# Kernel optimization log

Measured on AMD Instinct MI355X. Metric: run time of the kernel, lower is better.

Reference implementation:

```python
import jax, jax.numpy as jnp
import numpy as np


def _coord1d(n):
    # make_coord: grid-center coordinates in (-1, 1)
    return -1.0 + 1.0 / n + (2.0 / n) * jnp.arange(n, dtype=jnp.float32)


def _conv1x1(x, w, b):
    # 1x1 conv == channel matmul. x: [B,C,H,W], w: [O,C], b: [O]
    return jnp.einsum('bchw,oc->bohw', x, w) + b[None, :, None, None]


def setup_inputs() -> dict:
    key = jax.random.key(0)
    ks = jax.random.split(key, 8)
    B, C, h, w = 2, 64, 96, 96
    d = 256
    Cin = (C + 2) * 4 + 2  # 266
    s = lambda k, shp, fan: (jax.random.normal(k, shp, jnp.float32) / np.sqrt(fan)).astype(jnp.float32)
    return {
        'feat': jax.random.normal(ks[0], (B, C, h, w), jnp.float32),
        'w00': s(ks[1], (d, Cin), Cin), 'b00': jnp.zeros((d,), jnp.float32),
        'w1': s(ks[2], (d, d), d), 'b1': jnp.zeros((d,), jnp.float32),
        'w2': s(ks[3], (3, d), d), 'b2': jnp.zeros((3,), jnp.float32),
        'ws1': s(ks[4], (C, C), C), 'bs1': jnp.zeros((C,), jnp.float32),
        'ws2': s(ks[5], (3, C), C), 'bs2': jnp.zeros((3,), jnp.float32),
        'target_h': 384, 'target_w': 384,
    }


def reference(feat, w00, b00, w1, b1, w2, b2, ws1, bs1, ws2, bs2, target_h, target_w):
    B, C, h, w = feat.shape
    H, W = int(target_h), int(target_w)
    # HR query coordinates, shared across batch. cy along height (dim0), cx along width (dim1)
    cy = jnp.broadcast_to(_coord1d(H)[:, None], (H, W))
    cx = jnp.broadcast_to(_coord1d(W)[None, :], (H, W))
    rx = 1.0 / h  # = 2/h/2, half-pixel radius along height
    ry = 1.0 / w
    eps_shift = 1e-6

    def nearest(c, n):
        # grid_sample nearest, align_corners=False: unnormalize then round (half-to-even, as nearbyint)
        u = ((c + 1.0) * n - 1.0) / 2.0
        return jnp.clip(jnp.round(u).astype(jnp.int32), 0, n - 1)

    rel_coords, feat_s, areas = [], [], []
    for vx in (-1.0, 1.0):
        for vy in (-1.0, 1.0):
            sy = jnp.clip(cy + vx * rx + eps_shift, -1.0 + 1e-6, 1.0 - 1e-6)
            sx = jnp.clip(cx + vy * ry + eps_shift, -1.0 + 1e-6, 1.0 - 1e-6)
            iy = nearest(sy, h)  # [H,W]
            ix = nearest(sx, w)
            feat_s.append(feat[:, :, iy, ix])  # [B,C,H,W] gather
            # nearest-sampled LR pixel-center coords (what grid_sample(pos_lr,...) returns)
            old_y = -1.0 + 1.0 / h + (2.0 / h) * iy.astype(jnp.float32)
            old_x = -1.0 + 1.0 / w + (2.0 / w) * ix.astype(jnp.float32)
            rel_y = (cy - old_y) * h
            rel_x = (cx - old_x) * w
            rel_coords.append(jnp.stack([rel_y, rel_x], 0))  # [2,H,W]
            areas.append(jnp.abs(rel_y * rel_x) + 1e-9)

    tot = areas[0] + areas[1] + areas[2] + areas[3]
    # LIIF area swap: 0<->3, 1<->2
    areas = [areas[3], areas[2], areas[1], areas[0]]
    feat_s = [f * (a / tot)[None, None] for f, a in zip(feat_s, areas)]

    scale_h, scale_w = H / h, W / w
    cell_h = (2.0 / H) * max(scale_h / 4.0, 1.0) * h
    cell_w = (2.0 / W) * max(scale_w / 4.0, 1.0) * w
    rel_cell = jnp.broadcast_to(
        jnp.array([cell_h, cell_w], jnp.float32)[None, :, None, None], (B, 2, H, W))
    rels = jnp.broadcast_to(jnp.concatenate(rel_coords, 0)[None], (B, 8, H, W))
    grid = jnp.concatenate([rels, *feat_s, rel_cell], axis=1)  # [B,266,H,W]

    x = _conv1x1(grid, w00, b00)
    ret = _conv1x1(jax.nn.gelu(_conv1x1(x, w1, b1), approximate=False), w2, b2)

    # shortcut branch: 1x1 MLP on LR feat, then bilinear border sample at coord
    sc = _conv1x1(jax.nn.relu(_conv1x1(feat, ws1, bs1)), ws2, bs2)  # [B,3,h,w]
    uy = ((cy + 1.0) * h - 1.0) / 2.0
    ux = ((cx + 1.0) * w - 1.0) / 2.0
    y0 = jnp.floor(uy)
    x0 = jnp.floor(ux)
    wy = uy - y0
    wx = ux - x0
    y0i = jnp.clip(y0.astype(jnp.int32), 0, h - 1)
    y1i = jnp.clip(y0.astype(jnp.int32) + 1, 0, h - 1)
    x0i = jnp.clip(x0.astype(jnp.int32), 0, w - 1)
    x1i = jnp.clip(x0.astype(jnp.int32) + 1, 0, w - 1)
    samp = (sc[:, :, y0i, x0i] * ((1 - wy) * (1 - wx))[None, None]
            + sc[:, :, y0i, x1i] * ((1 - wy) * wx)[None, None]
            + sc[:, :, y1i, x0i] * (wy * (1 - wx))[None, None]
            + sc[:, :, y1i, x1i] * (wy * wx)[None, None])
    return ret + samp
```

## Files before the change

kernel.cpp:

```cpp
#include <hip/hip_runtime.h>

typedef __bf16 bf16x8 __attribute__((ext_vector_type(8)));
typedef __bf16 bf16x4 __attribute__((ext_vector_type(4)));
typedef float f32x4 __attribute__((ext_vector_type(4)));

namespace {
constexpr int Bn = 2, Cn = 64, hn = 96, wn = 96, Hn = 384, Wn = 384;
constexpr int CIN = 266;
constexpr int TM = 64;
constexpr int SP = 296;
constexpr int L1_FRAGS = 9 * 16 * 64;
constexpr int L2_FRAGS = 8 * 16 * 64;
constexpr int L3_FRAGS = 8 * 64;
constexpr int N_FRAGS = L1_FRAGS + L2_FRAGS + L3_FRAGS;
constexpr int SC_OFF_BYTES = N_FRAGS * 16;
constexpr int B1EFF_OFF_BYTES = SC_OFF_BYTES + Bn * 3 * hn * wn * 4;
constexpr int FEATT_OFF_BYTES = B1EFF_OFF_BYTES + 1024;
constexpr int FRAG_BLOCKS = N_FRAGS / 256;
constexpr int SC_BLOCKS = (Bn * hn * wn) / 256;
}

__global__ void prep_all(const float* __restrict__ w00, const float* __restrict__ w1,
                         const float* __restrict__ w2, const float* __restrict__ b00,
                         const float* __restrict__ b1,
                         const float* __restrict__ feat, const float* __restrict__ ws1,
                         const float* __restrict__ bs1, const float* __restrict__ ws2,
                         const float* __restrict__ bs2,
                         __bf16* __restrict__ wb, float* __restrict__ b1eff,
                         float* __restrict__ sc, float* __restrict__ featT)
{
    const int bid = blockIdx.x;
    if (bid < FRAG_BLOCKS) {
        const int f = bid * 256 + threadIdx.x;
        bf16x8 v;
        if (f < L1_FRAGS) {
            const int k0 = f >> 10;
            const int mb = (f >> 6) & 15;
            const int l  = f & 63;
            const int m  = mb * 16 + (l & 15);
            const int kb = k0 * 32 + (l >> 4) * 8;
#pragma unroll
            for (int j = 0; j < 8; j++)
                v[j] = (kb + j < CIN) ? (__bf16)w00[m * CIN + kb + j] : (__bf16)0.f;
        } else if (f < L1_FRAGS + L2_FRAGS) {
            const int g = f - L1_FRAGS;
            const int k0 = g >> 10;
            const int mb = (g >> 6) & 15;
            const int l  = g & 63;
            const int m  = mb * 16 + (l & 15);
            const int kb = k0 * 32 + (l >> 4) * 8;
#pragma unroll
            for (int j = 0; j < 8; j++) v[j] = (__bf16)w1[m * 256 + kb + j];
        } else {
            const int g = f - (L1_FRAGS + L2_FRAGS);
            const int k0 = g >> 6;
            const int l  = g & 63;
            const int m  = l & 15;
            const int kb = k0 * 32 + (l >> 4) * 8;
#pragma unroll
            for (int j = 0; j < 8; j++)
                v[j] = (m < 3) ? (__bf16)w2[m * 256 + kb + j] : (__bf16)0.f;
        }
        *(bf16x8*)(wb + f * 8) = v;
        return;
    }
    if (bid == FRAG_BLOCKS) {
        __shared__ float cb[256];
        const int o = threadIdx.x;
        cb[o] = b00[o] + 0.5f * (w00[o * CIN + 264] + w00[o * CIN + 265]);
        __syncthreads();
        float v = b1[o];
#pragma unroll 4
        for (int k = 0; k < 256; k++) v = fmaf(w1[o * 256 + k], cb[k], v);
        b1eff[o] = v;
        return;
    }
    const int t = (bid - FRAG_BLOCKS - 1) * 256 + threadIdx.x;
    if (t >= Bn * hn * wn) return;
    const int b = t / (hn * wn);
    const int yx = t % (hn * wn);
    const float* fp = feat + b * Cn * hn * wn + yx;
    float f[Cn];
#pragma unroll
    for (int c = 0; c < Cn; c++) f[c] = fp[c * hn * wn];
    {
        float* ft = featT + t * Cn;
#pragma unroll
        for (int c4 = 0; c4 < Cn / 4; c4++)
            *(f32x4*)&ft[c4 * 4] =
                (f32x4){f[4 * c4], f[4 * c4 + 1], f[4 * c4 + 2], f[4 * c4 + 3]};
    }
    float o0 = bs2[0], o1 = bs2[1], o2 = bs2[2];
#pragma unroll 1
    for (int co = 0; co < Cn; co += 4) {
        float v0 = bs1[co], v1 = bs1[co + 1], v2 = bs1[co + 2], v3 = bs1[co + 3];
        const float* wr = ws1 + co * Cn;
#pragma unroll
        for (int ci = 0; ci < Cn; ci++) {
            const float fv = f[ci];
            v0 = fmaf(wr[ci], fv, v0);
            v1 = fmaf(wr[Cn + ci], fv, v1);
            v2 = fmaf(wr[2 * Cn + ci], fv, v2);
            v3 = fmaf(wr[3 * Cn + ci], fv, v3);
        }
        v0 = fmaxf(v0, 0.f); v1 = fmaxf(v1, 0.f); v2 = fmaxf(v2, 0.f); v3 = fmaxf(v3, 0.f);
#pragma unroll
        for (int u = 0; u < 4; u++) {
            const float vv = (u == 0) ? v0 : (u == 1) ? v1 : (u == 2) ? v2 : v3;
            o0 = fmaf(ws2[co + u], vv, o0);
            o1 = fmaf(ws2[Cn + co + u], vv, o1);
            o2 = fmaf(ws2[2 * Cn + co + u], vv, o2);
        }
    }
    sc[(b * 3 + 0) * hn * wn + yx] = o0;
    sc[(b * 3 + 1) * hn * wn + yx] = o1;
    sc[(b * 3 + 2) * hn * wn + yx] = o2;
}

__device__ __forceinline__ float gelu_fast(float x) {
    const float d0 = -2.302118074f;
    const float d1 = -0.1029453754f;
    float t = x * x;
    float a = x * fmaf(t, d1, d0);
    float e = __builtin_amdgcn_exp2f(a);
    return x * __builtin_amdgcn_rcpf(1.f + e);
}

__device__ __forceinline__ bf16x4 pack4(f32x4 x) {
    bf16x4 v;
    v[0] = (__bf16)x[0]; v[1] = (__bf16)x[1]; v[2] = (__bf16)x[2]; v[3] = (__bf16)x[3];
    return v;
}


#define MF(A, B, C) __builtin_amdgcn_mfma_f32_16x16x32_bf16((A), (B), (C), 0, 0, 0)

#define GSTEP(k0, W0, W1, W2, W3) do {                                          \
    const bf16x8 g0 = *(const bf16x8*)&Abuf[     lane16][(k0) * 32 + quad * 8]; \
    const bf16x8 g1 = *(const bf16x8*)&Abuf[16 + lane16][(k0) * 32 + quad * 8]; \
    const bf16x8 g2 = *(const bf16x8*)&Abuf[32 + lane16][(k0) * 32 + quad * 8]; \
    const bf16x8 g3 = *(const bf16x8*)&Abuf[48 + lane16][(k0) * 32 + quad * 8]; \
    a00 = MF(W0, g0, a00); a01 = MF(W1, g0, a01); a02 = MF(W2, g0, a02); a03 = MF(W3, g0, a03); \
    a10 = MF(W0, g1, a10); a11 = MF(W1, g1, a11); a12 = MF(W2, g1, a12); a13 = MF(W3, g1, a13); \
    a20 = MF(W0, g2, a20); a21 = MF(W1, g2, a21); a22 = MF(W2, g2, a22); a23 = MF(W3, g2, a23); \
    a30 = MF(W0, g3, a30); a31 = MF(W1, g3, a31); a32 = MF(W2, g3, a32); a33 = MF(W3, g3, a33); \
} while (0)

#define LDW(W0, W1, W2, W3, src, kk) do {             \
    W0 = (src)[((kk) * 16 + mb0 + 0) * 64 + lane];    \
    W1 = (src)[((kk) * 16 + mb0 + 1) * 64 + lane];    \
    W2 = (src)[((kk) * 16 + mb0 + 2) * 64 + lane];    \
    W3 = (src)[((kk) * 16 + mb0 + 3) * 64 + lane];    \
} while (0)

#define ZACC4(n) a##n##0 = zf; a##n##1 = zf; a##n##2 = zf; a##n##3 = zf

__global__ __launch_bounds__(256, 3) void liif_main(
    const float* __restrict__ featT, const float* __restrict__ b1eff,
    const float* __restrict__ b2v, const __bf16* __restrict__ wb,
    const float* __restrict__ sc, float* __restrict__ out)
{
    __shared__ __align__(16) __bf16 Abuf[TM][SP];

    const int t = threadIdx.x;
    const int wv = t >> 6;
    const int lane = t & 63;
    const int lane16 = lane & 15;
    const int quad = lane >> 4;
    const int mb0 = wv * 4;

    constexpr int NWG = Bn * Hn * (Wn / TM);
    const int lt = (blockIdx.x & 7) * (NWG / 8) + (blockIdx.x >> 3);
    constexpr int TPR = Wn / TM;
    const int tx = lt % TPR;
    const int Y = (lt / TPR) % Hn;
    const int b = lt / (TPR * Hn);
    const int X0 = tx * TM;

    const float cy = -1.f + 1.f / Hn + (2.f / Hn) * (float)Y;

    const bf16x8* wf1 = (const bf16x8*)wb;
    const bf16x8* wf2 = wf1 + L1_FRAGS;
    const bf16x8* w2f = wf1 + (L1_FRAGS + L2_FRAGS);

    bf16x8 wE0, wE1, wE2, wE3, wO0, wO1, wO2, wO3;
    LDW(wE0, wE1, wE2, wE3, wf1, 0);
    LDW(wO0, wO1, wO2, wO3, wf1, 1);

    {
        const int p = lane;
        const int j = wv;
        const int X = X0 + p;
        const float cx = -1.f + 1.f / Wn + (2.f / Wn) * (float)X;
        float relyv[2], relxv[2];
        int iyy[2], ixx[2];
#pragma unroll
        for (int c2 = 0; c2 < 2; c2++) {
            const float v = c2 ? 1.f : -1.f;
            float sy = fminf(fmaxf(cy + v * (1.f / hn) + 1e-6f, -1.f + 1e-6f), 1.f - 1e-6f);
            float uy = ((sy + 1.f) * hn - 1.f) * 0.5f;
            int iy = min(max((int)rintf(uy), 0), hn - 1);
            float oy = -1.f + 1.f / hn + (2.f / hn) * (float)iy;
            relyv[c2] = (cy - oy) * hn; iyy[c2] = iy;
            float sx = fminf(fmaxf(cx + v * (1.f / wn) + 1e-6f, -1.f + 1e-6f), 1.f - 1e-6f);
            float ux = ((sx + 1.f) * wn - 1.f) * 0.5f;
            int ix = min(max((int)rintf(ux), 0), wn - 1);
            float ox = -1.f + 1.f / wn + (2.f / wn) * (float)ix;
            relxv[c2] = (cx - ox) * wn; ixx[c2] = ix;
        }
        float area[4];
#pragma unroll
        for (int c = 0; c < 4; c++)
            area[c] = fabsf(relyv[(c >> 1) & 1] * relxv[c & 1]) + 1e-9f;
        const float tot = area[0] + area[1] + area[2] + area[3];
        const float wj = area[3 - j] / tot;

        if (j == 0) {
            bf16x8 v;
#pragma unroll
            for (int c = 0; c < 4; c++) {
                v[2 * c] = (__bf16)relyv[(c >> 1) & 1];
                v[2 * c + 1] = (__bf16)relxv[c & 1];
            }
            *(bf16x8*)&Abuf[p][0] = v;
        }
        const float* fb = featT + ((b * hn + iyy[(j >> 1) & 1]) * wn + ixx[j & 1]) * Cn;
#pragma unroll
        for (int c8 = 0; c8 < 8; c8++) {
            const f32x4 u0 = *(const f32x4*)&fb[c8 * 8];
            const f32x4 u1 = *(const f32x4*)&fb[c8 * 8 + 4];
            bf16x8 v;
            v[0] = (__bf16)(u0[0] * wj); v[1] = (__bf16)(u0[1] * wj);
            v[2] = (__bf16)(u0[2] * wj); v[3] = (__bf16)(u0[3] * wj);
            v[4] = (__bf16)(u1[0] * wj); v[5] = (__bf16)(u1[1] * wj);
            v[6] = (__bf16)(u1[2] * wj); v[7] = (__bf16)(u1[3] * wj);
            *(bf16x8*)&Abuf[p][8 + 64 * j + c8 * 8] = v;
        }
        if (j == 3) {
            bf16x8 z;
#pragma unroll
            for (int cc = 0; cc < 8; cc++) z[cc] = (__bf16)0.f;
            *(bf16x8*)&Abuf[p][264] = z;
            *(bf16x8*)&Abuf[p][272] = z;
            *(bf16x8*)&Abuf[p][280] = z;
        }
    }
    __syncthreads();

    const f32x4 zf = (f32x4){0.f, 0.f, 0.f, 0.f};
    f32x4 a00, a01, a02, a03, a10, a11, a12, a13;
    f32x4 a20, a21, a22, a23, a30, a31, a32, a33;
    ZACC4(0); ZACC4(1); ZACC4(2); ZACC4(3);

    GSTEP(0, wE0, wE1, wE2, wE3); LDW(wE0, wE1, wE2, wE3, wf1, 2);
    GSTEP(1, wO0, wO1, wO2, wO3); LDW(wO0, wO1, wO2, wO3, wf1, 3);
    GSTEP(2, wE0, wE1, wE2, wE3); LDW(wE0, wE1, wE2, wE3, wf1, 4);
    GSTEP(3, wO0, wO1, wO2, wO3); LDW(wO0, wO1, wO2, wO3, wf1, 5);
    GSTEP(4, wE0, wE1, wE2, wE3); LDW(wE0, wE1, wE2, wE3, wf1, 6);
    GSTEP(5, wO0, wO1, wO2, wO3); LDW(wO0, wO1, wO2, wO3, wf1, 7);
    GSTEP(6, wE0, wE1, wE2, wE3); LDW(wE0, wE1, wE2, wE3, wf1, 8);
    GSTEP(7, wO0, wO1, wO2, wO3); LDW(wO0, wO1, wO2, wO3, wf2, 0);
    GSTEP(8, wE0, wE1, wE2, wE3); LDW(wE0, wE1, wE2, wE3, wf2, 1);

    __syncthreads();
    {
        const int ch0 = mb0 * 16 + quad * 4;
        *(bf16x4*)&Abuf[     lane16][ch0     ] = pack4(a00);
        *(bf16x4*)&Abuf[16 + lane16][ch0     ] = pack4(a10);
        *(bf16x4*)&Abuf[32 + lane16][ch0     ] = pack4(a20);
        *(bf16x4*)&Abuf[48 + lane16][ch0     ] = pack4(a30);
        *(bf16x4*)&Abuf[     lane16][ch0 + 16] = pack4(a01);
        *(bf16x4*)&Abuf[16 + lane16][ch0 + 16] = pack4(a11);
        *(bf16x4*)&Abuf[32 + lane16][ch0 + 16] = pack4(a21);
        *(bf16x4*)&Abuf[48 + lane16][ch0 + 16] = pack4(a31);
        *(bf16x4*)&Abuf[     lane16][ch0 + 32] = pack4(a02);
        *(bf16x4*)&Abuf[16 + lane16][ch0 + 32] = pack4(a12);
        *(bf16x4*)&Abuf[32 + lane16][ch0 + 32] = pack4(a22);
        *(bf16x4*)&Abuf[48 + lane16][ch0 + 32] = pack4(a32);
        *(bf16x4*)&Abuf[     lane16][ch0 + 48] = pack4(a03);
        *(bf16x4*)&Abuf[16 + lane16][ch0 + 48] = pack4(a13);
        *(bf16x4*)&Abuf[32 + lane16][ch0 + 48] = pack4(a23);
        *(bf16x4*)&Abuf[48 + lane16][ch0 + 48] = pack4(a33);
    }
    __syncthreads();

    ZACC4(0); ZACC4(1); ZACC4(2); ZACC4(3);

    GSTEP(0, wO0, wO1, wO2, wO3); LDW(wO0, wO1, wO2, wO3, wf2, 2);
    GSTEP(1, wE0, wE1, wE2, wE3); LDW(wE0, wE1, wE2, wE3, wf2, 3);
    GSTEP(2, wO0, wO1, wO2, wO3); LDW(wO0, wO1, wO2, wO3, wf2, 4);
    GSTEP(3, wE0, wE1, wE2, wE3); LDW(wE0, wE1, wE2, wE3, wf2, 5);
    GSTEP(4, wO0, wO1, wO2, wO3); LDW(wO0, wO1, wO2, wO3, wf2, 6);
    GSTEP(5, wE0, wE1, wE2, wE3); LDW(wE0, wE1, wE2, wE3, wf2, 7);
    GSTEP(6, wO0, wO1, wO2, wO3); wO0 = w2f[0 * 64 + lane];
    GSTEP(7, wE0, wE1, wE2, wE3); wE0 = w2f[1 * 64 + lane];

    __syncthreads();
    {
        const int ch0 = mb0 * 16 + quad * 4;
        const f32x4 bi0 = *(const f32x4*)&b1eff[ch0];
        const f32x4 bi1 = *(const f32x4*)&b1eff[ch0 + 16];
        const f32x4 bi2 = *(const f32x4*)&b1eff[ch0 + 32];
        const f32x4 bi3 = *(const f32x4*)&b1eff[ch0 + 48];
#define GEL4(x, bi) { bf16x4 v; v[0] = (__bf16)gelu_fast((x)[0] + (bi)[0]); \
        v[1] = (__bf16)gelu_fast((x)[1] + (bi)[1]); \
        v[2] = (__bf16)gelu_fast((x)[2] + (bi)[2]); \
        v[3] = (__bf16)gelu_fast((x)[3] + (bi)[3]); vv = v; }
        bf16x4 vv;
        GEL4(a00, bi0); *(bf16x4*)&Abuf[     lane16][ch0     ] = vv;
        GEL4(a10, bi0); *(bf16x4*)&Abuf[16 + lane16][ch0     ] = vv;
        GEL4(a20, bi0); *(bf16x4*)&Abuf[32 + lane16][ch0     ] = vv;
        GEL4(a30, bi0); *(bf16x4*)&Abuf[48 + lane16][ch0     ] = vv;
        GEL4(a01, bi1); *(bf16x4*)&Abuf[     lane16][ch0 + 16] = vv;
        GEL4(a11, bi1); *(bf16x4*)&Abuf[16 + lane16][ch0 + 16] = vv;
        GEL4(a21, bi1); *(bf16x4*)&Abuf[32 + lane16][ch0 + 16] = vv;
        GEL4(a31, bi1); *(bf16x4*)&Abuf[48 + lane16][ch0 + 16] = vv;
        GEL4(a02, bi2); *(bf16x4*)&Abuf[     lane16][ch0 + 32] = vv;
        GEL4(a12, bi2); *(bf16x4*)&Abuf[16 + lane16][ch0 + 32] = vv;
        GEL4(a22, bi2); *(bf16x4*)&Abuf[32 + lane16][ch0 + 32] = vv;
        GEL4(a32, bi2); *(bf16x4*)&Abuf[48 + lane16][ch0 + 32] = vv;
        GEL4(a03, bi3); *(bf16x4*)&Abuf[     lane16][ch0 + 48] = vv;
        GEL4(a13, bi3); *(bf16x4*)&Abuf[16 + lane16][ch0 + 48] = vv;
        GEL4(a23, bi3); *(bf16x4*)&Abuf[32 + lane16][ch0 + 48] = vv;
        GEL4(a33, bi3); *(bf16x4*)&Abuf[48 + lane16][ch0 + 48] = vv;
#undef GEL4
    }
    __syncthreads();

    f32x4 acc3 = zf;
#define YF(k0) (*(const bf16x8*)&Abuf[wv * 16 + lane16][(k0) * 32 + quad * 8])
    acc3 = MF(wO0, YF(0), acc3); wO0 = w2f[2 * 64 + lane];
    acc3 = MF(wE0, YF(1), acc3); wE0 = w2f[3 * 64 + lane];
    acc3 = MF(wO0, YF(2), acc3); wO0 = w2f[4 * 64 + lane];
    acc3 = MF(wE0, YF(3), acc3); wE0 = w2f[5 * 64 + lane];
    acc3 = MF(wO0, YF(4), acc3); wO0 = w2f[6 * 64 + lane];
    acc3 = MF(wE0, YF(5), acc3); wE0 = w2f[7 * 64 + lane];
    acc3 = MF(wO0, YF(6), acc3);
    acc3 = MF(wE0, YF(7), acc3);
#undef YF

    if (quad == 0) {
        const int pix = wv * 16 + lane16;
        const int X = X0 + pix;
        const float uy = ((cy + 1.f) * hn - 1.f) * 0.5f;
        const float fy = floorf(uy);
        const float wy = uy - fy;
        const int y0i = min(max((int)fy, 0), hn - 1);
        const int y1i = min(max((int)fy + 1, 0), hn - 1);
        const float cx = -1.f + 1.f / Wn + (2.f / Wn) * (float)X;
        const float ux = ((cx + 1.f) * wn - 1.f) * 0.5f;
        const float fx = floorf(ux);
        const float wx = ux - fx;
        const int x0i = min(max((int)fx, 0), wn - 1);
        const int x1i = min(max((int)fx + 1, 0), wn - 1);
        const float w00b = (1.f - wy) * (1.f - wx), w01b = (1.f - wy) * wx;
        const float w10b = wy * (1.f - wx), w11b = wy * wx;
#pragma unroll
        for (int r = 0; r < 3; r++) {
            const float* scb = sc + (b * 3 + r) * (hn * wn);
            const float samp = scb[y0i * wn + x0i] * w00b + scb[y0i * wn + x1i] * w01b
                             + scb[y1i * wn + x0i] * w10b + scb[y1i * wn + x1i] * w11b;
            out[((b * 3 + r) * Hn + Y) * Wn + X] = acc3[r] + b2v[r] + samp;
        }
    }
}

extern "C" void kernel_launch(void* const* d_in, const int* in_sizes, int n_in,
                              void* d_out, int out_size, void* d_ws, size_t ws_size,
                              hipStream_t stream)
{
    const float* feat = (const float*)d_in[0];
    const float* w00  = (const float*)d_in[1];
    const float* b00  = (const float*)d_in[2];
    const float* w1   = (const float*)d_in[3];
    const float* b1   = (const float*)d_in[4];
    const float* w2   = (const float*)d_in[5];
    const float* b2   = (const float*)d_in[6];
    const float* ws1  = (const float*)d_in[7];
    const float* bs1  = (const float*)d_in[8];
    const float* ws2  = (const float*)d_in[9];
    const float* bs2  = (const float*)d_in[10];
    float* out = (float*)d_out;

    __bf16* wb    = (__bf16*)d_ws;
    float* scbuf  = (float*)((char*)d_ws + SC_OFF_BYTES);
    float* b1eff  = (float*)((char*)d_ws + B1EFF_OFF_BYTES);
    float* featT  = (float*)((char*)d_ws + FEATT_OFF_BYTES);

    prep_all<<<FRAG_BLOCKS + 1 + SC_BLOCKS, 256, 0, stream>>>(
        w00, w1, w2, b00, b1, feat, ws1, bs1, ws2, bs2, wb, b1eff, scbuf, featT);
    liif_main<<<Bn * Hn * (Wn / TM), 256, 0, stream>>>(featT, b1eff, b2, wb, scbuf, out);
}
```

Baseline: 207.0 us.

## Process two pixel tiles per workgroup, prefetching second tile's gather during first

```diff
diff --git a/kernel.cpp b/kernel.cpp
--- a/kernel.cpp
+++ b/kernel.cpp
@@ -153,7 +153,120 @@
     W3 = (src)[((kk) * 16 + mb0 + 3) * 64 + lane];    \
 } while (0)
 
-#define ZACC4(n) a##n##0 = zf; a##n##1 = zf; a##n##2 = zf; a##n##3 = zf
+#define ZACCALL do { a00 = zf; a01 = zf; a02 = zf; a03 = zf; \
+    a10 = zf; a11 = zf; a12 = zf; a13 = zf;                   \
+    a20 = zf; a21 = zf; a22 = zf; a23 = zf;                   \
+    a30 = zf; a31 = zf; a32 = zf; a33 = zf; } while (0)
+
+#define L1_SEC do {                                                   \
+    GSTEP(0, wE0, wE1, wE2, wE3); LDW(wE0, wE1, wE2, wE3, wf1, 2);    \
+    GSTEP(1, wO0, wO1, wO2, wO3); LDW(wO0, wO1, wO2, wO3, wf1, 3);    \
+    GSTEP(2, wE0, wE1, wE2, wE3); LDW(wE0, wE1, wE2, wE3, wf1, 4);    \
+    GSTEP(3, wO0, wO1, wO2, wO3); LDW(wO0, wO1, wO2, wO3, wf1, 5);    \
+    GSTEP(4, wE0, wE1, wE2, wE3); LDW(wE0, wE1, wE2, wE3, wf1, 6);    \
+    GSTEP(5, wO0, wO1, wO2, wO3); LDW(wO0, wO1, wO2, wO3, wf1, 7);    \
+    GSTEP(6, wE0, wE1, wE2, wE3); LDW(wE0, wE1, wE2, wE3, wf1, 8);    \
+    GSTEP(7, wO0, wO1, wO2, wO3); LDW(wO0, wO1, wO2, wO3, wf2, 0);    \
+    GSTEP(8, wE0, wE1, wE2, wE3); LDW(wE0, wE1, wE2, wE3, wf2, 1);    \
+} while (0)
+
+#define L2_SEC do {                                                   \
+    GSTEP(0, wO0, wO1, wO2, wO3); LDW(wO0, wO1, wO2, wO3, wf2, 2);    \
+    GSTEP(1, wE0, wE1, wE2, wE3); LDW(wE0, wE1, wE2, wE3, wf2, 3);    \
+    GSTEP(2, wO0, wO1, wO2, wO3); LDW(wO0, wO1, wO2, wO3, wf2, 4);    \
+    GSTEP(3, wE0, wE1, wE2, wE3); LDW(wE0, wE1, wE2, wE3, wf2, 5);    \
+    GSTEP(4, wO0, wO1, wO2, wO3); LDW(wO0, wO1, wO2, wO3, wf2, 6);    \
+    GSTEP(5, wE0, wE1, wE2, wE3); LDW(wE0, wE1, wE2, wE3, wf2, 7);    \
+    GSTEP(6, wO0, wO1, wO2, wO3); wO0 = w2f[0 * 64 + lane];           \
+    GSTEP(7, wE0, wE1, wE2, wE3); wE0 = w2f[1 * 64 + lane];           \
+} while (0)
+
+#define YF(k0) (*(const bf16x8*)&Abuf[wv * 16 + lane16][(k0) * 32 + quad * 8])
+#define L3_SEC do {                                                   \
+    acc3 = zf;                                                        \
+    acc3 = MF(wO0, YF(0), acc3); wO0 = w2f[2 * 64 + lane];            \
+    acc3 = MF(wE0, YF(1), acc3); wE0 = w2f[3 * 64 + lane];            \
+    acc3 = MF(wO0, YF(2), acc3); wO0 = w2f[4 * 64 + lane];            \
+    acc3 = MF(wE0, YF(3), acc3); wE0 = w2f[5 * 64 + lane];            \
+    acc3 = MF(wO0, YF(4), acc3); wO0 = w2f[6 * 64 + lane];            \
+    acc3 = MF(wE0, YF(5), acc3); wE0 = w2f[7 * 64 + lane];            \
+    acc3 = MF(wO0, YF(6), acc3);                                      \
+    acc3 = MF(wE0, YF(7), acc3);                                      \
+} while (0)
+
+#define EP1_STORE do {                                                \
+    const int ch0 = mb0 * 16 + quad * 4;                              \
+    *(bf16x4*)&Abuf[     lane16][ch0     ] = pack4(a00);              \
+    *(bf16x4*)&Abuf[16 + lane16][ch0     ] = pack4(a10);              \
+    *(bf16x4*)&Abuf[32 + lane16][ch0     ] = pack4(a20);              \
+    *(bf16x4*)&Abuf[48 + lane16][ch0     ] = pack4(a30);              \
+    *(bf16x4*)&Abuf[     lane16][ch0 + 16] = pack4(a01);              \
+    *(bf16x4*)&Abuf[16 + lane16][ch0 + 16] = pack4(a11);              \
+    *(bf16x4*)&Abuf[32 + lane16][ch0 + 16] = pack4(a21);              \
+    *(bf16x4*)&Abuf[48 + lane16][ch0 + 16] = pack4(a31);              \
+    *(bf16x4*)&Abuf[     lane16][ch0 + 32] = pack4(a02);              \
+    *(bf16x4*)&Abuf[16 + lane16][ch0 + 32] = pack4(a12);              \
+    *(bf16x4*)&Abuf[32 + lane16][ch0 + 32] = pack4(a22);              \
+    *(bf16x4*)&Abuf[48 + lane16][ch0 + 32] = pack4(a32);              \
+    *(bf16x4*)&Abuf[     lane16][ch0 + 48] = pack4(a03);              \
+    *(bf16x4*)&Abuf[16 + lane16][ch0 + 48] = pack4(a13);              \
+    *(bf16x4*)&Abuf[32 + lane16][ch0 + 48] = pack4(a23);              \
+    *(bf16x4*)&Abuf[48 + lane16][ch0 + 48] = pack4(a33);              \
+} while (0)
+
+#define GEL4(x, bi) { bf16x4 v_; v_[0] = (__bf16)gelu_fast((x)[0] + (bi)[0]); \
+    v_[1] = (__bf16)gelu_fast((x)[1] + (bi)[1]); \
+    v_[2] = (__bf16)gelu_fast((x)[2] + (bi)[2]); \
+    v_[3] = (__bf16)gelu_fast((x)[3] + (bi)[3]); vv = v_; }
+
+#define EP2_STORE do {                                                \
+    const int ch0 = mb0 * 16 + quad * 4;                              \
+    const f32x4 bi0 = *(const f32x4*)&b1eff[ch0];                     \
+    const f32x4 bi1 = *(const f32x4*)&b1eff[ch0 + 16];                \
+    const f32x4 bi2 = *(const f32x4*)&b1eff[ch0 + 32];                \
+    const f32x4 bi3 = *(const f32x4*)&b1eff[ch0 + 48];                \
+    bf16x4 vv;                                                        \
+    GEL4(a00, bi0); *(bf16x4*)&Abuf[     lane16][ch0     ] = vv;      \
+    GEL4(a10, bi0); *(bf16x4*)&Abuf[16 + lane16][ch0     ] = vv;      \
+    GEL4(a20, bi0); *(bf16x4*)&Abuf[32 + lane16][ch0     ] = vv;      \
+    GEL4(a30, bi0); *(bf16x4*)&Abuf[48 + lane16][ch0     ] = vv;      \
+    GEL4(a01, bi1); *(bf16x4*)&Abuf[     lane16][ch0 + 16] = vv;      \
+    GEL4(a11, bi1); *(bf16x4*)&Abuf[16 + lane16][ch0 + 16] = vv;      \
+    GEL4(a21, bi1); *(bf16x4*)&Abuf[32 + lane16][ch0 + 16] = vv;      \
+    GEL4(a31, bi1); *(bf16x4*)&Abuf[48 + lane16][ch0 + 16] = vv;      \
+    GEL4(a02, bi2); *(bf16x4*)&Abuf[     lane16][ch0 + 32] = vv;      \
+    GEL4(a12, bi2); *(bf16x4*)&Abuf[16 + lane16][ch0 + 32] = vv;      \
+    GEL4(a22, bi2); *(bf16x4*)&Abuf[32 + lane16][ch0 + 32] = vv;      \
+    GEL4(a32, bi2); *(bf16x4*)&Abuf[48 + lane16][ch0 + 32] = vv;      \
+    GEL4(a03, bi3); *(bf16x4*)&Abuf[     lane16][ch0 + 48] = vv;      \
+    GEL4(a13, bi3); *(bf16x4*)&Abuf[16 + lane16][ch0 + 48] = vv;      \
+    GEL4(a23, bi3); *(bf16x4*)&Abuf[32 + lane16][ch0 + 48] = vv;      \
+    GEL4(a33, bi3); *(bf16x4*)&Abuf[48 + lane16][ch0 + 48] = vv;      \
+} while (0)
+
+#define OUT_EPI(cy_, Y_, X0_, b_) do { if (quad == 0) {                              \
+    const int pix = wv * 16 + lane16;                                                \
+    const int X = (X0_) + pix;                                                       \
+    const float uy = (((cy_) + 1.f) * hn - 1.f) * 0.5f;                              \
+    const float fy = floorf(uy);                                                     \
+    const float wy = uy - fy;                                                        \
+    const int y0i = min(max((int)fy, 0), hn - 1);                                    \
+    const int y1i = min(max((int)fy + 1, 0), hn - 1);                                \
+    const float cx_ = -1.f + 1.f / Wn + (2.f / Wn) * (float)X;                       \
+    const float ux = ((cx_ + 1.f) * wn - 1.f) * 0.5f;                                \
+    const float fx = floorf(ux);                                                     \
+    const float wx = ux - fx;                                                        \
+    const int x0i = min(max((int)fx, 0), wn - 1);                                    \
+    const int x1i = min(max((int)fx + 1, 0), wn - 1);                                \
+    const float w00b = (1.f - wy) * (1.f - wx), w01b = (1.f - wy) * wx;              \
+    const float w10b = wy * (1.f - wx), w11b = wy * wx;                              \
+    _Pragma("unroll")                                                                \
+    for (int r = 0; r < 3; r++) {                                                    \
+        const float* scb = sc + ((b_) * 3 + r) * (hn * wn);                          \
+        const float samp = scb[y0i * wn + x0i] * w00b + scb[y0i * wn + x1i] * w01b   \
+                         + scb[y1i * wn + x0i] * w10b + scb[y1i * wn + x1i] * w11b;  \
+        out[(((b_) * 3 + r) * Hn + (Y_)) * Wn + X] = acc3[r] + b2v[r] + samp;        \
+    } } } while (0)
 
 __global__ __launch_bounds__(256, 3) void liif_main(
     const float* __restrict__ featT, const float* __restrict__ b1eff,
@@ -169,15 +282,21 @@
     const int quad = lane >> 4;
     const int mb0 = wv * 4;
 
-    constexpr int NWG = Bn * Hn * (Wn / TM);
-    const int lt = (blockIdx.x & 7) * (NWG / 8) + (blockIdx.x >> 3);
+    constexpr int NWG2 = Bn * Hn * (Wn / TM) / 2;
+    const int q = (blockIdx.x & 7) * (NWG2 / 8) + (blockIdx.x >> 3);
     constexpr int TPR = Wn / TM;
-    const int tx = lt % TPR;
-    const int Y = (lt / TPR) % Hn;
-    const int b = lt / (TPR * Hn);
-    const int X0 = tx * TM;
-
-    const float cy = -1.f + 1.f / Hn + (2.f / Hn) * (float)Y;
+    const int ltA = q * 2, ltB = q * 2 + 1;
+    const int txA = ltA % TPR;
+    const int YA = (ltA / TPR) % Hn;
+    const int bA = ltA / (TPR * Hn);
+    const int X0A = txA * TM;
+    const int txB = ltB % TPR;
+    const int YB = (ltB / TPR) % Hn;
+    const int bB = ltB / (TPR * Hn);
+    const int X0B = txB * TM;
+
+    const float cyA = -1.f + 1.f / Hn + (2.f / Hn) * (float)YA;
+    const float cyB = -1.f + 1.f / Hn + (2.f / Hn) * (float)YB;
 
     const bf16x8* wf1 = (const bf16x8*)wb;
     const bf16x8* wf2 = wf1 + L1_FRAGS;
@@ -190,18 +309,18 @@
     {
         const int p = lane;
         const int j = wv;
-        const int X = X0 + p;
+        const int X = X0A + p;
         const float cx = -1.f + 1.f / Wn + (2.f / Wn) * (float)X;
         float relyv[2], relxv[2];
         int iyy[2], ixx[2];
 #pragma unroll
         for (int c2 = 0; c2 < 2; c2++) {
             const float v = c2 ? 1.f : -1.f;
-            float sy = fminf(fmaxf(cy + v * (1.f / hn) + 1e-6f, -1.f + 1e-6f), 1.f - 1e-6f);
+            float sy = fminf(fmaxf(cyA + v * (1.f / hn) + 1e-6f, -1.f + 1e-6f), 1.f - 1e-6f);
             float uy = ((sy + 1.f) * hn - 1.f) * 0.5f;
             int iy = min(max((int)rintf(uy), 0), hn - 1);
             float oy = -1.f + 1.f / hn + (2.f / hn) * (float)iy;
-            relyv[c2] = (cy - oy) * hn; iyy[c2] = iy;
+            relyv[c2] = (cyA - oy) * hn; iyy[c2] = iy;
             float sx = fminf(fmaxf(cx + v * (1.f / wn) + 1e-6f, -1.f + 1e-6f), 1.f - 1e-6f);
             float ux = ((sx + 1.f) * wn - 1.f) * 0.5f;
             int ix = min(max((int)rintf(ux), 0), wn - 1);
@@ -224,7 +343,7 @@
             }
             *(bf16x8*)&Abuf[p][0] = v;
         }
-        const float* fb = featT + ((b * hn + iyy[(j >> 1) & 1]) * wn + ixx[j & 1]) * Cn;
+        const float* fb = featT + ((bA * hn + iyy[(j >> 1) & 1]) * wn + ixx[j & 1]) * Cn;
 #pragma unroll
         for (int c8 = 0; c8 < 8; c8++) {
             const f32x4 u0 = *(const f32x4*)&fb[c8 * 8];
@@ -250,119 +369,118 @@
     const f32x4 zf = (f32x4){0.f, 0.f, 0.f, 0.f};
     f32x4 a00, a01, a02, a03, a10, a11, a12, a13;
     f32x4 a20, a21, a22, a23, a30, a31, a32, a33;
-    ZACC4(0); ZACC4(1); ZACC4(2); ZACC4(3);
-
-    GSTEP(0, wE0, wE1, wE2, wE3); LDW(wE0, wE1, wE2, wE3, wf1, 2);
-    GSTEP(1, wO0, wO1, wO2, wO3); LDW(wO0, wO1, wO2, wO3, wf1, 3);
-    GSTEP(2, wE0, wE1, wE2, wE3); LDW(wE0, wE1, wE2, wE3, wf1, 4);
-    GSTEP(3, wO0, wO1, wO2, wO3); LDW(wO0, wO1, wO2, wO3, wf1, 5);
-    GSTEP(4, wE0, wE1, wE2, wE3); LDW(wE0, wE1, wE2, wE3, wf1, 6);
-    GSTEP(5, wO0, wO1, wO2, wO3); LDW(wO0, wO1, wO2, wO3, wf1, 7);
-    GSTEP(6, wE0, wE1, wE2, wE3); LDW(wE0, wE1, wE2, wE3, wf1, 8);
-    GSTEP(7, wO0, wO1, wO2, wO3); LDW(wO0, wO1, wO2, wO3, wf2, 0);
-    GSTEP(8, wE0, wE1, wE2, wE3); LDW(wE0, wE1, wE2, wE3, wf2, 1);
-
-    __syncthreads();
+    f32x4 acc3;
+    ZACCALL;
+
+    L1_SEC;
+
+    float ryB0, ryB1, rxB0, rxB1, wjB;
+    const float* fbB;
     {
-        const int ch0 = mb0 * 16 + quad * 4;
-        *(bf16x4*)&Abuf[     lane16][ch0     ] = pack4(a00);
-        *(bf16x4*)&Abuf[16 + lane16][ch0     ] = pack4(a10);
-        *(bf16x4*)&Abuf[32 + lane16][ch0     ] = pack4(a20);
-        *(bf16x4*)&Abuf[48 + lane16][ch0     ] = pack4(a30);
-        *(bf16x4*)&Abuf[     lane16][ch0 + 16] = pack4(a01);
-        *(bf16x4*)&Abuf[16 + lane16][ch0 + 16] = pack4(a11);
-        *(bf16x4*)&Abuf[32 + lane16][ch0 + 16] = pack4(a21);
-        *(bf16x4*)&Abuf[48 + lane16][ch0 + 16] = pack4(a31);
-        *(bf16x4*)&Abuf[     lane16][ch0 + 32] = pack4(a02);
-        *(bf16x4*)&Abuf[16 + lane16][ch0 + 32] = pack4(a12);
-        *(bf16x4*)&Abuf[32 + lane16][ch0 + 32] = pack4(a22);
-        *(bf16x4*)&Abuf[48 + lane16][ch0 + 32] = pack4(a32);
-        *(bf16x4*)&Abuf[     lane16][ch0 + 48] = pack4(a03);
-        *(bf16x4*)&Abuf[16 + lane16][ch0 + 48] = pack4(a13);
-        *(bf16x4*)&Abuf[32 + lane16][ch0 + 48] = pack4(a23);
-        *(bf16x4*)&Abuf[48 + lane16][ch0 + 48] = pack4(a33);
-    }
-    __syncthreads();
-
-    ZACC4(0); ZACC4(1); ZACC4(2); ZACC4(3);
-
-    GSTEP(0, wO0, wO1, wO2, wO3); LDW(wO0, wO1, wO2, wO3, wf2, 2);
-    GSTEP(1, wE0, wE1, wE2, wE3); LDW(wE0, wE1, wE2, wE3, wf2, 3);
-    GSTEP(2, wO0, wO1, wO2, wO3); LDW(wO0, wO1, wO2, wO3, wf2, 4);
-    GSTEP(3, wE0, wE1, wE2, wE3); LDW(wE0, wE1, wE2, wE3, wf2, 5);
-    GSTEP(4, wO0, wO1, wO2, wO3); LDW(wO0, wO1, wO2, wO3, wf2, 6);
-    GSTEP(5, wE0, wE1, wE2, wE3); LDW(wE0, wE1, wE2, wE3, wf2, 7);
-    GSTEP(6, wO0, wO1, wO2, wO3); wO0 = w2f[0 * 64 + lane];
-    GSTEP(7, wE0, wE1, wE2, wE3); wE0 = w2f[1 * 64 + lane];
-
-    __syncthreads();
+        const float cx = -1.f + 1.f / Wn + (2.f / Wn) * (float)(X0B + lane);
+        float relyv[2], relxv[2];
+        int iyy[2], ixx[2];
+#pragma unroll
+        for (int c2 = 0; c2 < 2; c2++) {
+            const float v = c2 ? 1.f : -1.f;
+            float sy = fminf(fmaxf(cyB + v * (1.f / hn) + 1e-6f, -1.f + 1e-6f), 1.f - 1e-6f);
+            float uy = ((sy + 1.f) * hn - 1.f) * 0.5f;
+            int iy = min(max((int)rintf(uy), 0), hn - 1);
+            float oy = -1.f + 1.f / hn + (2.f / hn) * (float)iy;
+            relyv[c2] = (cyB - oy) * hn; iyy[c2] = iy;
+            float sx = fminf(fmaxf(cx + v * (1.f / wn) + 1e-6f, -1.f + 1e-6f), 1.f - 1e-6f);
+            float ux = ((sx + 1.f) * wn - 1.f) * 0.5f;
+            int ix = min(max((int)rintf(ux), 0), wn - 1);
+            float ox = -1.f + 1.f / wn + (2.f / wn) * (float)ix;
+            relxv[c2] = (cx - ox) * wn; ixx[c2] = ix;
+        }
+        float area[4];
+#pragma unroll
+        for (int c = 0; c < 4; c++)
+            area[c] = fabsf(relyv[(c >> 1) & 1] * relxv[c & 1]) + 1e-9f;
+        const float tot = area[0] + area[1] + area[2] + area[3];
+        wjB = area[3 - wv] / tot;
+        ryB0 = relyv[0]; ryB1 = relyv[1]; rxB0 = relxv[0]; rxB1 = relxv[1];
+        fbB = featT + ((bB * hn + iyy[(wv >> 1) & 1]) * wn + ixx[wv & 1]) * Cn;
+    }
+
+    __syncthreads();
+    EP1_STORE;
+    __syncthreads();
+
+    ZACCALL;
+    L2_SEC;
+
+    __syncthreads();
+    EP2_STORE;
+    __syncthreads();
+
+    const f32x4 uB0  = *(const f32x4*)&fbB[0];
+    const f32x4 uB1  = *(const f32x4*)&fbB[4];
+    const f32x4 uB2  = *(const f32x4*)&fbB[8];
+    const f32x4 uB3  = *(const f32x4*)&fbB[12];
+    const f32x4 uB4  = *(const f32x4*)&fbB[16];
+    const f32x4 uB5  = *(const f32x4*)&fbB[20];
+    const f32x4 uB6  = *(const f32x4*)&fbB[24];
+    const f32x4 uB7  = *(const f32x4*)&fbB[28];
+    const f32x4 uB8  = *(const f32x4*)&fbB[32];
+    const f32x4 uB9  = *(const f32x4*)&fbB[36];
+    const f32x4 uB10 = *(const f32x4*)&fbB[40];
+    const f32x4 uB11 = *(const f32x4*)&fbB[44];
+    const f32x4 uB12 = *(const f32x4*)&fbB[48];
+    const f32x4 uB13 = *(const f32x4*)&fbB[52];
+    const f32x4 uB14 = *(const f32x4*)&fbB[56];
+    const f32x4 uB15 = *(const f32x4*)&fbB[60];
+
+    L3_SEC;
+    LDW(wE0, wE1, wE2, wE3, wf1, 0);
+    LDW(wO0, wO1, wO2, wO3, wf1, 1);
+    OUT_EPI(cyA, YA, X0A, bA);
+    __syncthreads();
+
     {
-        const int ch0 = mb0 * 16 + quad * 4;
-        const f32x4 bi0 = *(const f32x4*)&b1eff[ch0];
-        const f32x4 bi1 = *(const f32x4*)&b1eff[ch0 + 16];
-        const f32x4 bi2 = *(const f32x4*)&b1eff[ch0 + 32];
-        const f32x4 bi3 = *(const f32x4*)&b1eff[ch0 + 48];
-#define GEL4(x, bi) { bf16x4 v; v[0] = (__bf16)gelu_fast((x)[0] + (bi)[0]); \
-        v[1] = (__bf16)gelu_fast((x)[1] + (bi)[1]); \
-        v[2] = (__bf16)gelu_fast((x)[2] + (bi)[2]); \
-        v[3] = (__bf16)gelu_fast((x)[3] + (bi)[3]); vv = v; }
-        bf16x4 vv;
-        GEL4(a00, bi0); *(bf16x4*)&Abuf[     lane16][ch0     ] = vv;
-        GEL4(a10, bi0); *(bf16x4*)&Abuf[16 + lane16][ch0     ] = vv;
-        GEL4(a20, bi0); *(bf16x4*)&Abuf[32 + lane16][ch0     ] = vv;
-        GEL4(a30, bi0); *(bf16x4*)&Abuf[48 + lane16][ch0     ] = vv;
-        GEL4(a01, bi1); *(bf16x4*)&Abuf[     lane16][ch0 + 16] = vv;
-        GEL4(a11, bi1); *(bf16x4*)&Abuf[16 + lane16][ch0 + 16] = vv;
-        GEL4(a21, bi1); *(bf16x4*)&Abuf[32 + lane16][ch0 + 16] = vv;
-        GEL4(a31, bi1); *(bf16x4*)&Abuf[48 + lane16][ch0 + 16] = vv;
-        GEL4(a02, bi2); *(bf16x4*)&Abuf[     lane16][ch0 + 32] = vv;
-        GEL4(a12, bi2); *(bf16x4*)&Abuf[16 + lane16][ch0 + 32] = vv;
-        GEL4(a22, bi2); *(bf16x4*)&Abuf[32 + lane16][ch0 + 32] = vv;
-        GEL4(a32, bi2); *(bf16x4*)&Abuf[48 + lane16][ch0 + 32] = vv;
-        GEL4(a03, bi3); *(bf16x4*)&Abuf[     lane16][ch0 + 48] = vv;
-        GEL4(a13, bi3); *(bf16x4*)&Abuf[16 + lane16][ch0 + 48] = vv;
-        GEL4(a23, bi3); *(bf16x4*)&Abuf[32 + lane16][ch0 + 48] = vv;
-        GEL4(a33, bi3); *(bf16x4*)&Abuf[48 + lane16][ch0 + 48] = vv;
-#undef GEL4
-    }
-    __syncthreads();
-
-    f32x4 acc3 = zf;
-#define YF(k0) (*(const bf16x8*)&Abuf[wv * 16 + lane16][(k0) * 32 + quad * 8])
-    acc3 = MF(wO0, YF(0), acc3); wO0 = w2f[2 * 64 + lane];
-    acc3 = MF(wE0, YF(1), acc3); wE0 = w2f[3 * 64 + lane];
-    acc3 = MF(wO0, YF(2), acc3); wO0 = w2f[4 * 64 + lane];
-    acc3 = MF(wE0, YF(3), acc3); wE0 = w2f[5 * 64 + lane];
-    acc3 = MF(wO0, YF(4), acc3); wO0 = w2f[6 * 64 + lane];
-    acc3 = MF(wE0, YF(5), acc3); wE0 = w2f[7 * 64 + lane];
-    acc3 = MF(wO0, YF(6), acc3);
-    acc3 = MF(wE0, YF(7), acc3);
-#undef YF
-
-    if (quad == 0) {
-        const int pix = wv * 16 + lane16;
-        const int X = X0 + pix;
-        const float uy = ((cy + 1.f) * hn - 1.f) * 0.5f;
-        const float fy = floorf(uy);
-        const float wy = uy - fy;
-        const int y0i = min(max((int)fy, 0), hn - 1);
-        const int y1i = min(max((int)fy + 1, 0), hn - 1);
-        const float cx = -1.f + 1.f / Wn + (2.f / Wn) * (float)X;
-        const float ux = ((cx + 1.f) * wn - 1.f) * 0.5f;
-        const float fx = floorf(ux);
-        const float wx = ux - fx;
-        const int x0i = min(max((int)fx, 0), wn - 1);
-        const int x1i = min(max((int)fx + 1, 0), wn - 1);
-        const float w00b = (1.f - wy) * (1.f - wx), w01b = (1.f - wy) * wx;
-        const float w10b = wy * (1.f - wx), w11b = wy * wx;
-#pragma unroll
-        for (int r = 0; r < 3; r++) {
-            const float* scb = sc + (b * 3 + r) * (hn * wn);
-            const float samp = scb[y0i * wn + x0i] * w00b + scb[y0i * wn + x1i] * w01b
-                             + scb[y1i * wn + x0i] * w10b + scb[y1i * wn + x1i] * w11b;
-            out[((b * 3 + r) * Hn + Y) * Wn + X] = acc3[r] + b2v[r] + samp;
-        }
-    }
+        if (wv == 0) {
+            bf16x8 v;
+            v[0] = (__bf16)ryB0; v[1] = (__bf16)rxB0;
+            v[2] = (__bf16)ryB0; v[3] = (__bf16)rxB1;
+            v[4] = (__bf16)ryB1; v[5] = (__bf16)rxB0;
+            v[6] = (__bf16)ryB1; v[7] = (__bf16)rxB1;
+            *(bf16x8*)&Abuf[lane][0] = v;
+        }
+#define STB(c8, U0, U1) { bf16x8 v;                                       \
+        v[0] = (__bf16)((U0)[0] * wjB); v[1] = (__bf16)((U0)[1] * wjB);   \
+        v[2] = (__bf16)((U0)[2] * wjB); v[3] = (__bf16)((U0)[3] * wjB);   \
+        v[4] = (__bf16)((U1)[0] * wjB); v[5] = (__bf16)((U1)[1] * wjB);   \
+        v[6] = (__bf16)((U1)[2] * wjB); v[7] = (__bf16)((U1)[3] * wjB);   \
+        *(bf16x8*)&Abuf[lane][8 + 64 * wv + (c8) * 8] = v; }
+        STB(0, uB0,  uB1);  STB(1, uB2,  uB3);
+        STB(2, uB4,  uB5);  STB(3, uB6,  uB7);
+        STB(4, uB8,  uB9);  STB(5, uB10, uB11);
+        STB(6, uB12, uB13); STB(7, uB14, uB15);
+#undef STB
+        if (wv == 3) {
+            bf16x8 z;
+#pragma unroll
+            for (int cc = 0; cc < 8; cc++) z[cc] = (__bf16)0.f;
+            *(bf16x8*)&Abuf[lane][264] = z;
+            *(bf16x8*)&Abuf[lane][272] = z;
+            *(bf16x8*)&Abuf[lane][280] = z;
+        }
+    }
+    __syncthreads();
+
+    ZACCALL;
+    L1_SEC;
+    __syncthreads();
+    EP1_STORE;
+    __syncthreads();
+    ZACCALL;
+    L2_SEC;
+    __syncthreads();
+    EP2_STORE;
+    __syncthreads();
+    L3_SEC;
+    OUT_EPI(cyB, YB, X0B, bB);
 }
 
 extern "C" void kernel_launch(void* const* d_in, const int* in_sizes, int n_in,
@@ -389,5 +507,5 @@
 
     prep_all<<<FRAG_BLOCKS + 1 + SC_BLOCKS, 256, 0, stream>>>(
         w00, w1, w2, b00, b1, feat, ws1, bs1, ws2, bs2, wb, b1eff, scbuf, featT);
-    liif_main<<<Bn * Hn * (Wn / TM), 256, 0, stream>>>(featT, b1eff, b2, wb, scbuf, out);
+    liif_main<<<Bn * Hn * (Wn / TM) / 2, 256, 0, stream>>>(featT, b1eff, b2, wb, scbuf, out);
 }
```

Measured after the change: 361.0 us. +74.4%, slower.
